# Optimization experiments

Measured on AMD Instinct MI355X. Metric: run time of the kernel, lower is better.

## Reference

```python
import jax, jax.numpy as jnp
import numpy as np

N = 10000   # function nodes
E = 160000  # edges (avg in/out degree ~16)
C = 8       # hidden channels per function node (fix_hidden_channels=True)
B = 64      # batch
EPS = 1e-5


def setup_inputs() -> dict:
    key = jax.random.key(0)
    ks = jax.random.split(key, 6)
    x = jax.random.normal(ks[0], (B, E), jnp.float32)
    # xavier-ish scale for fan_in ~ avg_degree=16
    w1 = jax.random.normal(ks[1], (E, C), jnp.float32) * 0.25
    b1 = jnp.zeros((N, C), jnp.float32)
    w3 = jax.random.normal(ks[2], (E, C), jnp.float32) * 0.25
    b3 = jnp.zeros((E,), jnp.float32)
    gamma = jnp.ones((N, C), jnp.float32)
    beta = jnp.zeros((N, C), jnp.float32)
    edge_src = jax.random.randint(ks[3], (E,), 0, N, dtype=jnp.int32)
    edge_dst = jax.random.randint(ks[4], (E,), 0, N, dtype=jnp.int32)
    return dict(x=x, w1=w1, b1=b1, gamma=gamma, beta=beta, w3=w3, b3=b3,
                edge_src=edge_src, edge_dst=edge_dst)


def reference(x, w1, b1, gamma, beta, w3, b3, edge_src, edge_dst):
    # --- lin1: SparseLinear (E -> N*C); W1[e, (v,k)] != 0 iff v == dst(e) ---
    # out1[b, v, k] = sum_{e: dst(e)==v} x[b, e] * w1[e, k] + b1[v, k]
    vals = x.T[:, :, None] * w1[:, None, :]                    # [E, B, C]
    h = jax.ops.segment_sum(vals, edge_dst, num_segments=N)    # [N, B, C]
    h = jnp.transpose(h, (1, 0, 2)) + b1                       # [B, N, C]
    # --- GroupLayerNorm: normalize over each node's C-channel group ---
    mu = jnp.mean(h, axis=-1, keepdims=True)
    var = jnp.var(h, axis=-1, keepdims=True)
    h = (h - mu) * jax.lax.rsqrt(var + EPS) * gamma + beta
    # --- nonlin (ELU); dropout p=0 in eval mode -> identity ---
    h = jax.nn.elu(h)
    # --- lin3: SparseLinear (N*C -> E); W3[(v,k), e] != 0 iff v == src(e) ---
    # out[b, e] = sum_k h[b, src(e), k] * w3[e, k] + b3[e]
    g = h[:, edge_src, :]                                      # [B, E, C]
    out = jnp.einsum('bec,ec->be', g, w3) + b3                 # [B, E]
    # --- residual ---
    return out + x
```

## Files before the change

kernel.cpp:

```cpp
#include <hip/hip_runtime.h>

#define N_NODES 10000
#define N_EDGES 160000
#define NC 8
#define LN_EPS 1e-5f

typedef _Float16 h4_t __attribute__((ext_vector_type(4)));
typedef _Float16 h8_t __attribute__((ext_vector_type(8)));

__device__ __forceinline__ int swz(int e, int b) {
  return e * 64 + ((((b >> 2) ^ ((e >> 2) & 15)) << 2) | (b & 3));
}

__global__ void hist_kernel(const int* __restrict__ edst, int* __restrict__ cnt_dst) {
  const int e = blockIdx.x * 256 + threadIdx.x;
  if (e < N_EDGES) atomicAdd(&cnt_dst[edst[e]], 1);
}

__global__ void __launch_bounds__(1024) scan_kernel(
    const int* __restrict__ cnt, int* __restrict__ start, int* __restrict__ cur) {
  const int t = threadIdx.x;
  const int lane = t & 63;
  const int wid = t >> 6;
  const int lo = t * 10;
  const int hi = min(lo + 10, N_NODES);
  int s = 0;
  for (int i = lo; i < hi; ++i) s += cnt[i];
  const int own = s;
#pragma unroll
  for (int d = 1; d < 64; d <<= 1) {
    const int v = __shfl_up(s, d, 64);
    if (lane >= d) s += v;
  }
  __shared__ int wsum[16];
  if (lane == 63) wsum[wid] = s;
  __syncthreads();
  if (t == 0) {
    int acc = 0;
#pragma unroll
    for (int i = 0; i < 16; ++i) { acc += wsum[i]; wsum[i] = acc; }
  }
  __syncthreads();
  int base = (wid ? wsum[wid - 1] : 0) + s - own;
  for (int i = lo; i < hi; ++i) {
    start[i] = base;
    cur[i] = base;
    base += cnt[i];
  }
  if (t == 1023) start[N_NODES] = base;
}

__global__ void __launch_bounds__(256) prep_kernel(
    const float* __restrict__ x, const int* __restrict__ edst,
    const float* __restrict__ w1, int* __restrict__ cur_dst,
    _Float16* __restrict__ xT_d, _Float16* __restrict__ w1_h) {
  __shared__ float tile[64 * 64];
  __shared__ int pP[64];
  const int e0 = blockIdx.x * 64;
  const int t = threadIdx.x;

  if (t < 64) {
    const int e = e0 + t;
    const int p = atomicAdd(&cur_dst[edst[e]], 1);
    pP[t] = p;
    const float4* wp1 = (const float4*)(w1 + (size_t)e * NC);
    const float4 wa = wp1[0], wb = wp1[1];
    h8_t hw;
    hw[0] = (_Float16)wa.x; hw[1] = (_Float16)wa.y;
    hw[2] = (_Float16)wa.z; hw[3] = (_Float16)wa.w;
    hw[4] = (_Float16)wb.x; hw[5] = (_Float16)wb.y;
    hw[6] = (_Float16)wb.z; hw[7] = (_Float16)wb.w;
    *(h8_t*)&w1_h[(size_t)p * NC] = hw;
  }

  const int u = t & 15;
  const int row = t >> 4;
#pragma unroll
  for (int j = 0; j < 4; ++j) {
    const int b = j * 16 + row;
    const float4 xv = *(const float4*)&x[(size_t)b * N_EDGES + e0 + 4 * u];
    tile[swz(4 * u + 0, b)] = xv.x;
    tile[swz(4 * u + 1, b)] = xv.y;
    tile[swz(4 * u + 2, b)] = xv.z;
    tile[swz(4 * u + 3, b)] = xv.w;
  }
  __syncthreads();
#pragma unroll
  for (int j = 0; j < 4; ++j) {
    const int r = j * 16 + row;
    const float4 vv = *(const float4*)&tile[r * 64 + ((u ^ ((r >> 2) & 15)) << 2)];
    h4_t hv;
    hv[0] = (_Float16)vv.x; hv[1] = (_Float16)vv.y;
    hv[2] = (_Float16)vv.z; hv[3] = (_Float16)vv.w;
    *(h4_t*)&xT_d[(size_t)pP[r] * 64 + 4 * u] = hv;
  }
}

__global__ void __launch_bounds__(256) node_kernel(
    const _Float16* __restrict__ xT_d, const _Float16* __restrict__ w1_h,
    const float* __restrict__ b1, const float* __restrict__ gamma,
    const float* __restrict__ beta, const int* __restrict__ start_dst,
    _Float16* __restrict__ v) {
  const int n = blockIdx.x * 4 + (threadIdx.x >> 6);
  const int b = threadIdx.x & 63;

  float a[NC];
#pragma unroll
  for (int c = 0; c < NC; ++c) a[c] = 0.f;

  const int s0 = start_dst[n];
  const int s1 = start_dst[n + 1];
  int i = s0;
  for (; i + 4 <= s1; i += 4) {
    float xe[4];
#pragma unroll
    for (int k = 0; k < 4; ++k) xe[k] = (float)xT_d[(size_t)(i + k) * 64 + b];
    h8_t wl[4];
#pragma unroll
    for (int k = 0; k < 4; ++k) wl[k] = *(const h8_t*)&w1_h[(size_t)(i + k) * NC];
#pragma unroll
    for (int k = 0; k < 4; ++k) {
#pragma unroll
      for (int c = 0; c < NC; ++c) a[c] += xe[k] * (float)wl[k][c];
    }
  }
  for (; i < s1; ++i) {
    const float xe = (float)xT_d[(size_t)i * 64 + b];
    const h8_t wl = *(const h8_t*)&w1_h[(size_t)i * NC];
#pragma unroll
    for (int c = 0; c < NC; ++c) a[c] += xe * (float)wl[c];
  }

  const float4* b1p = (const float4*)(b1 + (size_t)n * NC);
  const float4 b1a = b1p[0], b1b = b1p[1];
  a[0] += b1a.x; a[1] += b1a.y; a[2] += b1a.z; a[3] += b1a.w;
  a[4] += b1b.x; a[5] += b1b.y; a[6] += b1b.z; a[7] += b1b.w;

  float mu = 0.f;
#pragma unroll
  for (int c = 0; c < NC; ++c) mu += a[c];
  mu *= 0.125f;
  float var = 0.f;
#pragma unroll
  for (int c = 0; c < NC; ++c) { a[c] -= mu; var += a[c] * a[c]; }
  var *= 0.125f;
  const float rs = rsqrtf(var + LN_EPS);

  const float4* gp = (const float4*)(gamma + (size_t)n * NC);
  const float4 ga = gp[0], gb = gp[1];
  const float4* bp = (const float4*)(beta + (size_t)n * NC);
  const float4 ba = bp[0], bb = bp[1];
  float w[NC];
  w[0] = a[0] * rs * ga.x + ba.x;  w[1] = a[1] * rs * ga.y + ba.y;
  w[2] = a[2] * rs * ga.z + ba.z;  w[3] = a[3] * rs * ga.w + ba.w;
  w[4] = a[4] * rs * gb.x + bb.x;  w[5] = a[5] * rs * gb.y + bb.y;
  w[6] = a[6] * rs * gb.z + bb.z;  w[7] = a[7] * rs * gb.w + bb.w;
#pragma unroll
  for (int c = 0; c < NC; ++c) w[c] = w[c] > 0.f ? w[c] : expm1f(w[c]);

  h8_t hv;
#pragma unroll
  for (int c = 0; c < NC; ++c) hv[c] = (_Float16)w[c];
  *(h8_t*)&v[(size_t)n * 512 + b * NC] = hv;
}

__global__ void __launch_bounds__(256) edge_kernel(
    const _Float16* __restrict__ v, const float* __restrict__ w3,
    const float* __restrict__ b3, const float* __restrict__ x,
    const int* __restrict__ esrc, float* __restrict__ out) {
  __shared__ float tile[64 * 64];
  const int e0 = blockIdx.x * 64;
  const int t = threadIdx.x;
  const int w = t >> 6;
  const int b = t & 63;
  const int u = t & 15;
  const int row = t >> 4;

  int sidx = 0;
  if (b < 16) sidx = esrc[e0 + w * 16 + b];

  h8_t hv[16];
#pragma unroll
  for (int r = 0; r < 16; ++r) {
    const int s = __shfl(sidx, r, 64);
    hv[r] = *(const h8_t*)&v[(size_t)s * 512 + b * NC];
  }
  const float4 bb = *(const float4*)&b3[e0 + 4 * u];
  float4 xb[4];
#pragma unroll
  for (int j = 0; j < 4; ++j) {
    const int bo = j * 16 + row;
    xb[j] = *(const float4*)&x[(size_t)bo * N_EDGES + e0 + 4 * u];
  }

#pragma unroll
  for (int r = 0; r < 16; ++r) {
    const float4* wp = (const float4*)(w3 + (size_t)(e0 + w * 16 + r) * NC);
    const float4 wa = wp[0], wb = wp[1];
    const float dot =
        (float)hv[r][0] * wa.x + (float)hv[r][1] * wa.y +
        (float)hv[r][2] * wa.z + (float)hv[r][3] * wa.w +
        (float)hv[r][4] * wb.x + (float)hv[r][5] * wb.y +
        (float)hv[r][6] * wb.z + (float)hv[r][7] * wb.w;
    tile[swz(w * 16 + r, b)] = dot;
  }
  __syncthreads();

#pragma unroll
  for (int j = 0; j < 4; ++j) {
    const int bo = j * 16 + row;
    const float o0 = tile[swz(4 * u + 0, bo)];
    const float o1 = tile[swz(4 * u + 1, bo)];
    const float o2 = tile[swz(4 * u + 2, bo)];
    const float o3 = tile[swz(4 * u + 3, bo)];
    float4 o;
    o.x = o0 + bb.x + xb[j].x;  o.y = o1 + bb.y + xb[j].y;
    o.z = o2 + bb.z + xb[j].z;  o.w = o3 + bb.w + xb[j].w;
    *(float4*)&out[(size_t)bo * N_EDGES + e0 + 4 * u] = o;
  }
}

extern "C" void kernel_launch(void* const* d_in, const int* in_sizes, int n_in,
                              void* d_out, int out_size, void* d_ws, size_t ws_size,
                              hipStream_t stream) {
  const float* x     = (const float*)d_in[0];
  const float* w1    = (const float*)d_in[1];
  const float* b1    = (const float*)d_in[2];
  const float* gamma = (const float*)d_in[3];
  const float* beta  = (const float*)d_in[4];
  const float* w3    = (const float*)d_in[5];
  const float* b3    = (const float*)d_in[6];
  const int* esrc    = (const int*)d_in[7];
  const int* edst    = (const int*)d_in[8];
  float* out = (float*)d_out;

  char* ws = (char*)d_ws;
  size_t off = 0;
  auto alloc = [&](size_t bytes) -> void* {
    void* p = ws + off;
    off += (bytes + 255) & ~(size_t)255;
    return p;
  };
  _Float16* xT_d   = (_Float16*)alloc((size_t)N_EDGES * 64 * 2);
  _Float16* w1_h   = (_Float16*)alloc((size_t)N_EDGES * NC * 2);
  _Float16* v      = (_Float16*)alloc((size_t)N_NODES * 512 * 2);
  int* cnt_dst     = (int*)alloc((size_t)N_NODES * 4);
  int* start_dst   = (int*)alloc((size_t)(N_NODES + 1) * 4);
  int* cur_dst     = (int*)alloc((size_t)N_NODES * 4);

  hipMemsetAsync(cnt_dst, 0, (size_t)N_NODES * 4, stream);

  hist_kernel<<<N_EDGES / 256, 256, 0, stream>>>(edst, cnt_dst);
  scan_kernel<<<1, 1024, 0, stream>>>(cnt_dst, start_dst, cur_dst);
  prep_kernel<<<N_EDGES / 64, 256, 0, stream>>>(x, edst, w1, cur_dst, xT_d, w1_h);
  node_kernel<<<N_NODES / 4, 256, 0, stream>>>(xT_d, w1_h, b1, gamma, beta,
                                               start_dst, v);
  edge_kernel<<<N_EDGES / 64, 256, 0, stream>>>(v, w3, b3, x, esrc, out);
}
```

Measured before the change: 187.5 us.

## Compute lin3 dot products in node kernel via src-sorted CSR, gather scalars per edge

Builds a second CSR keyed on edge source, permuting w3 into src order during prep. The node kernel now computes each outgoing edge's 8-channel dot product directly from its normalized activations and writes fp16 results per (edge, batch). The edge kernel then gathers one fp16 scalar instead of an 8-wide fp16 vector plus w3. This cuts edge-kernel gather traffic, but adds another histogram/scan/atomic pass, a 20 MB dotT buffer write, and more work in the node kernel.

```diff
diff --git a/kernel.cpp b/kernel.cpp
--- a/kernel.cpp
+++ b/kernel.cpp
@@ -12,48 +12,65 @@
   return e * 64 + ((((b >> 2) ^ ((e >> 2) & 15)) << 2) | (b & 3));
 }
 
-__global__ void hist_kernel(const int* __restrict__ edst, int* __restrict__ cnt_dst) {
+__global__ void hist_kernel(const int* __restrict__ edst,
+                            const int* __restrict__ esrc,
+                            int* __restrict__ cnt) {
   const int e = blockIdx.x * 256 + threadIdx.x;
-  if (e < N_EDGES) atomicAdd(&cnt_dst[edst[e]], 1);
+  if (e < N_EDGES) {
+    atomicAdd(&cnt[edst[e]], 1);
+    atomicAdd(&cnt[N_NODES + esrc[e]], 1);
+  }
 }
 
 __global__ void __launch_bounds__(1024) scan_kernel(
-    const int* __restrict__ cnt, int* __restrict__ start, int* __restrict__ cur) {
+    const int* __restrict__ cnt,
+    int* __restrict__ start_d, int* __restrict__ cur_d,
+    int* __restrict__ start_s, int* __restrict__ cur_s) {
+  __shared__ int wsum[16];
   const int t = threadIdx.x;
   const int lane = t & 63;
   const int wid = t >> 6;
   const int lo = t * 10;
   const int hi = min(lo + 10, N_NODES);
-  int s = 0;
-  for (int i = lo; i < hi; ++i) s += cnt[i];
-  const int own = s;
-#pragma unroll
-  for (int d = 1; d < 64; d <<= 1) {
-    const int v = __shfl_up(s, d, 64);
-    if (lane >= d) s += v;
-  }
-  __shared__ int wsum[16];
-  if (lane == 63) wsum[wid] = s;
-  __syncthreads();
-  if (t == 0) {
-    int acc = 0;
-#pragma unroll
-    for (int i = 0; i < 16; ++i) { acc += wsum[i]; wsum[i] = acc; }
-  }
-  __syncthreads();
-  int base = (wid ? wsum[wid - 1] : 0) + s - own;
-  for (int i = lo; i < hi; ++i) {
-    start[i] = base;
-    cur[i] = base;
-    base += cnt[i];
-  }
-  if (t == 1023) start[N_NODES] = base;
+#pragma unroll
+  for (int pass = 0; pass < 2; ++pass) {
+    const int* c = cnt + pass * N_NODES;
+    int* start = pass ? start_s : start_d;
+    int* cur = pass ? cur_s : cur_d;
+    int s = 0;
+    for (int i = lo; i < hi; ++i) s += c[i];
+    const int own = s;
+#pragma unroll
+    for (int d = 1; d < 64; d <<= 1) {
+      const int v = __shfl_up(s, d, 64);
+      if (lane >= d) s += v;
+    }
+    if (lane == 63) wsum[wid] = s;
+    __syncthreads();
+    if (t == 0) {
+      int acc = 0;
+#pragma unroll
+      for (int i = 0; i < 16; ++i) { acc += wsum[i]; wsum[i] = acc; }
+    }
+    __syncthreads();
+    int base = (wid ? wsum[wid - 1] : 0) + s - own;
+    for (int i = lo; i < hi; ++i) {
+      start[i] = base;
+      cur[i] = base;
+      base += c[i];
+    }
+    if (t == 1023) start[N_NODES] = base;
+    __syncthreads();
+  }
 }
 
 __global__ void __launch_bounds__(256) prep_kernel(
     const float* __restrict__ x, const int* __restrict__ edst,
-    const float* __restrict__ w1, int* __restrict__ cur_dst,
-    _Float16* __restrict__ xT_d, _Float16* __restrict__ w1_h) {
+    const int* __restrict__ esrc,
+    const float* __restrict__ w1, const float* __restrict__ w3,
+    int* __restrict__ cur_dst, int* __restrict__ cur_src,
+    _Float16* __restrict__ xT_d, _Float16* __restrict__ w1_h,
+    float* __restrict__ w3_p, int* __restrict__ qsrc) {
   __shared__ float tile[64 * 64];
   __shared__ int pP[64];
   const int e0 = blockIdx.x * 64;
@@ -71,6 +88,13 @@
     hw[4] = (_Float16)wb.x; hw[5] = (_Float16)wb.y;
     hw[6] = (_Float16)wb.z; hw[7] = (_Float16)wb.w;
     *(h8_t*)&w1_h[(size_t)p * NC] = hw;
+
+    const int q = atomicAdd(&cur_src[esrc[e]], 1);
+    qsrc[e] = q;
+    const float4* wp3 = (const float4*)(w3 + (size_t)e * NC);
+    float4* wd = (float4*)(w3_p + (size_t)q * NC);
+    wd[0] = wp3[0];
+    wd[1] = wp3[1];
   }
 
   const int u = t & 15;
@@ -100,7 +124,8 @@
     const _Float16* __restrict__ xT_d, const _Float16* __restrict__ w1_h,
     const float* __restrict__ b1, const float* __restrict__ gamma,
     const float* __restrict__ beta, const int* __restrict__ start_dst,
-    _Float16* __restrict__ v) {
+    const int* __restrict__ start_src, const float* __restrict__ w3_p,
+    _Float16* __restrict__ dotT) {
   const int n = blockIdx.x * 4 + (threadIdx.x >> 6);
   const int b = threadIdx.x & 63;
 
@@ -158,16 +183,38 @@
 #pragma unroll
   for (int c = 0; c < NC; ++c) w[c] = w[c] > 0.f ? w[c] : expm1f(w[c]);
 
-  h8_t hv;
-#pragma unroll
-  for (int c = 0; c < NC; ++c) hv[c] = (_Float16)w[c];
-  *(h8_t*)&v[(size_t)n * 512 + b * NC] = hv;
+  const int o0 = start_src[n];
+  const int o1 = start_src[n + 1];
+  int q = o0;
+  for (; q + 4 <= o1; q += 4) {
+    float4 wva[4], wvb[4];
+#pragma unroll
+    for (int k = 0; k < 4; ++k) {
+      const float4* wp = (const float4*)(w3_p + (size_t)(q + k) * NC);
+      wva[k] = wp[0]; wvb[k] = wp[1];
+    }
+#pragma unroll
+    for (int k = 0; k < 4; ++k) {
+      const float dot =
+          w[0] * wva[k].x + w[1] * wva[k].y + w[2] * wva[k].z + w[3] * wva[k].w +
+          w[4] * wvb[k].x + w[5] * wvb[k].y + w[6] * wvb[k].z + w[7] * wvb[k].w;
+      dotT[(size_t)(q + k) * 64 + b] = (_Float16)dot;
+    }
+  }
+  for (; q < o1; ++q) {
+    const float4* wp = (const float4*)(w3_p + (size_t)q * NC);
+    const float4 wa = wp[0], wb2 = wp[1];
+    const float dot =
+        w[0] * wa.x + w[1] * wa.y + w[2] * wa.z + w[3] * wa.w +
+        w[4] * wb2.x + w[5] * wb2.y + w[6] * wb2.z + w[7] * wb2.w;
+    dotT[(size_t)q * 64 + b] = (_Float16)dot;
+  }
 }
 
 __global__ void __launch_bounds__(256) edge_kernel(
-    const _Float16* __restrict__ v, const float* __restrict__ w3,
+    const _Float16* __restrict__ dotT, const int* __restrict__ qsrc,
     const float* __restrict__ b3, const float* __restrict__ x,
-    const int* __restrict__ esrc, float* __restrict__ out) {
+    float* __restrict__ out) {
   __shared__ float tile[64 * 64];
   const int e0 = blockIdx.x * 64;
   const int t = threadIdx.x;
@@ -176,14 +223,14 @@
   const int u = t & 15;
   const int row = t >> 4;
 
-  int sidx = 0;
-  if (b < 16) sidx = esrc[e0 + w * 16 + b];
-
-  h8_t hv[16];
+  int qi = 0;
+  if (b < 16) qi = qsrc[e0 + w * 16 + b];
+
+  _Float16 dv[16];
 #pragma unroll
   for (int r = 0; r < 16; ++r) {
-    const int s = __shfl(sidx, r, 64);
-    hv[r] = *(const h8_t*)&v[(size_t)s * 512 + b * NC];
+    const int q = __shfl(qi, r, 64);
+    dv[r] = dotT[(size_t)q * 64 + b];
   }
   const float4 bb = *(const float4*)&b3[e0 + 4 * u];
   float4 xb[4];
@@ -194,16 +241,7 @@
   }
 
 #pragma unroll
-  for (int r = 0; r < 16; ++r) {
-    const float4* wp = (const float4*)(w3 + (size_t)(e0 + w * 16 + r) * NC);
-    const float4 wa = wp[0], wb = wp[1];
-    const float dot =
-        (float)hv[r][0] * wa.x + (float)hv[r][1] * wa.y +
-        (float)hv[r][2] * wa.z + (float)hv[r][3] * wa.w +
-        (float)hv[r][4] * wb.x + (float)hv[r][5] * wb.y +
-        (float)hv[r][6] * wb.z + (float)hv[r][7] * wb.w;
-    tile[swz(w * 16 + r, b)] = dot;
-  }
+  for (int r = 0; r < 16; ++r) tile[swz(w * 16 + r, b)] = (float)dv[r];
   __syncthreads();
 
 #pragma unroll
@@ -243,17 +281,25 @@
   };
   _Float16* xT_d   = (_Float16*)alloc((size_t)N_EDGES * 64 * 2);
   _Float16* w1_h   = (_Float16*)alloc((size_t)N_EDGES * NC * 2);
-  _Float16* v      = (_Float16*)alloc((size_t)N_NODES * 512 * 2);
-  int* cnt_dst     = (int*)alloc((size_t)N_NODES * 4);
+  float*    w3_p   = (float*)alloc((size_t)N_EDGES * NC * 4);
+  _Float16* dotT   = (_Float16*)alloc((size_t)N_EDGES * 64 * 2);
+  int* qsrc        = (int*)alloc((size_t)N_EDGES * 4);
+  int* cnt         = (int*)alloc((size_t)2 * N_NODES * 4);
   int* start_dst   = (int*)alloc((size_t)(N_NODES + 1) * 4);
   int* cur_dst     = (int*)alloc((size_t)N_NODES * 4);
-
-  hipMemsetAsync(cnt_dst, 0, (size_t)N_NODES * 4, stream);
-
-  hist_kernel<<<N_EDGES / 256, 256, 0, stream>>>(edst, cnt_dst);
-  scan_kernel<<<1, 1024, 0, stream>>>(cnt_dst, start_dst, cur_dst);
-  prep_kernel<<<N_EDGES / 64, 256, 0, stream>>>(x, edst, w1, cur_dst, xT_d, w1_h);
+  int* start_src   = (int*)alloc((size_t)(N_NODES + 1) * 4);
+  int* cur_src     = (int*)alloc((size_t)N_NODES * 4);
+
+  hipMemsetAsync(cnt, 0, (size_t)2 * N_NODES * 4, stream);
+
+  hist_kernel<<<N_EDGES / 256, 256, 0, stream>>>(edst, esrc, cnt);
+  scan_kernel<<<1, 1024, 0, stream>>>(cnt, start_dst, cur_dst,
+                                      start_src, cur_src);
+  prep_kernel<<<N_EDGES / 64, 256, 0, stream>>>(x, edst, esrc, w1, w3,
+                                                cur_dst, cur_src,
+                                                xT_d, w1_h, w3_p, qsrc);
   node_kernel<<<N_NODES / 4, 256, 0, stream>>>(xT_d, w1_h, b1, gamma, beta,
-                                               start_dst, v);
-  edge_kernel<<<N_EDGES / 64, 256, 0, stream>>>(v, w3, b3, x, esrc, out);
-}
+                                               start_dst, start_src, w3_p,
+                                               dotT);
+  edge_kernel<<<N_EDGES / 64, 256, 0, stream>>>(dotT, qsrc, b3, x, out);
+}
```

Result: slower. 211.4 us (+12.7%).
